# Kernel tuning notes

Measured on AMD Instinct MI355X. Metric: run time of the kernel, lower is better.

The kernel has to match this reference:

```python
import jax, jax.numpy as jnp
import numpy as np

H, C = 5, 128          # heads, hidden_channels
NUM_GRAPHS = 500
N_NODES, N_EDGES = 20000, 320000


def gat_layer(x, edge_attr, src, dst, W, We, a_src, a_dst, a_edge, b):
    """PyG GATConv with edge_dim, add_self_loops=True, fill_value='mean', concat heads."""
    N = x.shape[0]
    ed = edge_attr.dtype
    # self-loop edge_attr = scatter-mean of incoming edge_attr per target node
    deg = jax.ops.segment_sum(jnp.ones((dst.shape[0],), ed), dst, num_segments=N)
    loop_attr = jax.ops.segment_sum(edge_attr, dst, num_segments=N) / jnp.maximum(deg, 1.0)[:, None]
    loop = jnp.arange(N, dtype=src.dtype)
    s = jnp.concatenate([src, loop])
    d = jnp.concatenate([dst, loop])
    ea = jnp.concatenate([edge_attr, loop_attr], axis=0)
    h = (x @ W).reshape(N, H, C)            # [N,H,C]
    e = (ea @ We).reshape(-1, H, C)         # [E2,H,C]
    a_l = (h * a_src).sum(-1)               # [N,H]
    a_r = (h * a_dst).sum(-1)               # [N,H]
    a_e = (e * a_edge).sum(-1)              # [E2,H]
    alpha = jax.nn.leaky_relu(a_l[s] + a_r[d] + a_e, 0.2)
    # segment softmax over destination neighborhoods
    amax = jax.ops.segment_max(alpha, d, num_segments=N)
    ex = jnp.exp(alpha - amax[d])
    denom = jax.ops.segment_sum(ex, d, num_segments=N)
    att = ex / (denom[d] + 1e-16)           # [E2,H]
    msg = h[s] * att[..., None]             # [E2,H,C]
    out = jax.ops.segment_sum(msg, d, num_segments=N).reshape(N, H * C)
    return out + b


def setup_inputs() -> dict:
    key = jax.random.key(0)
    ks = jax.random.split(key, 24)
    p = lambda k, sh: (jax.random.normal(k, sh, dtype=jnp.float32) * 0.05)
    inp = {
        "x": jax.random.normal(ks[0], (N_NODES, 43), dtype=jnp.float32),
        "edge_attr": jax.random.normal(ks[1], (N_EDGES, 10), dtype=jnp.float32),
        "W1": p(ks[2], (43, H * C)),   "We1": p(ks[3], (10, H * C)),
        "asrc1": p(ks[4], (H, C)), "adst1": p(ks[5], (H, C)), "aedge1": p(ks[6], (H, C)),
        "b1": jnp.zeros((H * C,), jnp.float32),
        "W2": p(ks[7], (H * C, H * C)), "We2": p(ks[8], (10, H * C)),
        "asrc2": p(ks[9], (H, C)), "adst2": p(ks[10], (H, C)), "aedge2": p(ks[11], (H, C)),
        "b2": jnp.zeros((H * C,), jnp.float32),
        "W3": p(ks[12], (H * C, H * C)), "We3": p(ks[13], (10, H * C)),
        "asrc3": p(ks[14], (H, C)), "adst3": p(ks[15], (H, C)), "aedge3": p(ks[16], (H, C)),
        "b3": jnp.zeros((H * C,), jnp.float32),
        "Wlin": p(ks[17], (H * C, 1)), "blin": jnp.zeros((1,), jnp.float32),
        "edge_index": jax.random.randint(ks[18], (2, N_EDGES), 0, N_NODES, dtype=jnp.int32),
        "batch": jnp.sort(jax.random.randint(ks[19], (N_NODES,), 0, NUM_GRAPHS, dtype=jnp.int32)),
    }
    return inp


def reference(x, edge_attr, W1, We1, asrc1, adst1, aedge1, b1,
              W2, We2, asrc2, adst2, aedge2, b2,
              W3, We3, asrc3, adst3, aedge3, b3,
              Wlin, blin, edge_index, batch):
    src, dst = edge_index[0], edge_index[1]
    h = jax.nn.relu(gat_layer(x, edge_attr, src, dst, W1, We1, asrc1, adst1, aedge1, b1))
    h = jax.nn.relu(gat_layer(h, edge_attr, src, dst, W2, We2, asrc2, adst2, aedge2, b2))
    h = gat_layer(h, edge_attr, src, dst, W3, We3, asrc3, adst3, aedge3, b3)
    # global mean pool over graphs
    cnt = jax.ops.segment_sum(jnp.ones((h.shape[0],), h.dtype), batch, num_segments=NUM_GRAPHS)
    pooled = jax.ops.segment_sum(h, batch, num_segments=NUM_GRAPHS) / jnp.maximum(cnt, 1.0)[:, None]
    return (pooled @ Wlin + blin).squeeze(-1)   # [NUM_GRAPHS]
```

## Files before the change

### kernel.cpp

```cpp
#include <hip/hip_runtime.h>

#define N_NODESC 20000
#define N_EDGESC 320000
#define HC 640
#define NGRAPH 500

typedef unsigned short u16;
typedef unsigned int u32;
typedef __attribute__((ext_vector_type(8))) short bf16x8;
typedef __attribute__((ext_vector_type(4))) float f32x4;

__device__ __forceinline__ float wred_sum(float v){
  #pragma unroll
  for(int o=32;o;o>>=1) v += __shfl_xor(v,o,64);
  return v;
}
__device__ __forceinline__ float lrelu(float x){ return x>0.f? x:0.2f*x; }

__device__ __forceinline__ u16 f2bf(float f){
  u32 u=__float_as_uint(f);
  u32 r=u+0x7FFFu+((u>>16)&1u);
  return (u16)(r>>16);
}
__device__ __forceinline__ float bf2f(u16 s){ return __uint_as_float(((u32)s)<<16); }
__device__ __forceinline__ float bflo(u32 w){ return __uint_as_float(w<<16); }
__device__ __forceinline__ float bfhi(u32 w){ return __uint_as_float(w&0xFFFF0000u); }

__device__ __forceinline__ void gload16(const void* g, void* l){
  __builtin_amdgcn_global_load_lds((const __attribute__((address_space(1))) void*)g,
                                   (__attribute__((address_space(3))) void*)l, 16, 0, 0);
}


__global__ void k_count(const int* __restrict__ dst, int* __restrict__ cnt){
  int i=blockIdx.x*blockDim.x+threadIdx.x;
  if(i>=N_EDGESC) return;
  atomicAdd(&cnt[dst[i]],1);
}

__global__ void k_scan(const int* __restrict__ cnt, int* __restrict__ rptr, int* __restrict__ pos){
  __shared__ int ps[1024];
  int t=threadIdx.x;
  const int CH=20;
  int beg=t*CH, end=min(beg+CH, N_NODESC);
  int s=0;
  for(int i=beg;i<end;i++) s+=cnt[i];
  ps[t]=s; __syncthreads();
  for(int off=1;off<1024;off<<=1){
    int v=(t>=off)? ps[t-off]:0;
    __syncthreads();
    ps[t]+=v;
    __syncthreads();
  }
  int base=ps[t]-s;
  for(int i=beg;i<end;i++){ rptr[i]=base; pos[i]=base; base+=cnt[i]; }
}

__global__ void k_scatter(const int* __restrict__ dst, int* __restrict__ pos,
                          int* __restrict__ eidx, int* __restrict__ dstC){
  int i=blockIdx.x*blockDim.x+threadIdx.x;
  if(i>=N_EDGESC) return;
  int d=dst[i];
  int j=atomicAdd(&pos[d],1);
  eidx[j]=i;
  dstC[j]=d;
}

__global__ void k_csr_edges(const int* __restrict__ eidx, const int* __restrict__ src,
                            const float* __restrict__ eattr,
                            int* __restrict__ srcE, float* __restrict__ eattrC){
  int j=blockIdx.x*blockDim.x+threadIdx.x;
  if(j>=N_EDGESC) return;
  int e=eidx[j];
  srcE[j]=src[e];
  const float* ep=&eattr[(size_t)e*10];
  float* op=&eattrC[(size_t)j*10];
  #pragma unroll
  for(int k=0;k<10;k++) op[k]=ep[k];
}

__global__ __launch_bounds__(256) void k_loop_attr(const float* __restrict__ eattrC,
    const int* __restrict__ rptr, const int* __restrict__ cnt,
    float* __restrict__ lattr){
  int tid=threadIdx.x, lane=tid&63;
  int n=blockIdx.x*4+(tid>>6);
  if(n>=N_NODESC) return;
  int beg=rptr[n], deg=cnt[n];
  float s[10]={0,0,0,0,0,0,0,0,0,0};
  for(int off=lane; off<deg; off+=64){
    const float* ep=&eattrC[(size_t)(beg+off)*10];
    #pragma unroll
    for(int k=0;k<10;k++) s[k]+=ep[k];
  }
  float inv=1.f/fmaxf((float)deg,1.f);
  #pragma unroll
  for(int k=0;k<10;k++){
    float tot=wred_sum(s[k]);
    if(lane==0) lattr[(size_t)n*10+k]=tot*inv;
  }
}


__global__ void k_conv_x(const float* __restrict__ x, u16* __restrict__ hi, u16* __restrict__ lo){
  int idx=blockIdx.x*blockDim.x+threadIdx.x;
  if(idx>=N_NODESC*64) return;
  int n=idx>>6, kk=idx&63;
  float v = kk<43 ? x[n*43+kk] : 0.f;
  u16 h=f2bf(v);
  hi[idx]=h; lo[idx]=f2bf(v-bf2f(h));
}

__global__ void k_conv_w3(const float* __restrict__ W0, const float* __restrict__ W1,
                          const float* __restrict__ W2,
                          u16* __restrict__ hi, u16* __restrict__ lo){
  const int R0=HC*64, R1=R0+HC*HC;
  const int TOT=R1+HC*HC;
  int idx=blockIdx.x*blockDim.x+threadIdx.x;
  if(idx>=TOT) return;
  const float* W; int local, KP, KL, base;
  if(idx<R0){ W=W0; local=idx; KP=64; KL=43; base=0; }
  else if(idx<R1){ W=W1; local=idx-R0; KP=HC; KL=HC; base=R0; }
  else { W=W2; local=idx-R1; KP=HC; KL=HC; base=R1; }
  int n=local/KP, kk=local-n*KP;
  float v = kk<KL ? W[(size_t)kk*HC+n] : 0.f;
  u16 h=f2bf(v);
  hi[base+local]=h;
  lo[base+local]=f2bf(v-bf2f(h));
}


__global__ void k_ve3(const float* __restrict__ We0, const float* __restrict__ ae0,
                      const float* __restrict__ We1, const float* __restrict__ ae1,
                      const float* __restrict__ We2, const float* __restrict__ ae2,
                      float* __restrict__ ve3){
  int t=threadIdx.x;
  if(t>=150) return;
  int L=t/50, r=t-50*L, k=r/5, h=r%5;
  const float* We = (L==0)?We0:(L==1)?We1:We2;
  const float* ae = (L==0)?ae0:(L==1)?ae1:ae2;
  float s=0.f;
  for(int c=0;c<128;c++) s += We[k*HC + h*128 + c]*ae[h*128+c];
  ve3[t]=s;
}

__global__ void k_cb(const float* __restrict__ bias, const float* __restrict__ wlin,
                     float* __restrict__ cb){
  int lane=threadIdx.x;
  float s=0.f;
  for(int c=lane;c<HC;c+=64) s+=bias[c]*wlin[c];
  s=wred_sum(s);
  if(lane==0) cb[0]=s;
}

__global__ __launch_bounds__(256) void k_edge_terms3(const float* __restrict__ eattrC,
    const float* __restrict__ lattr, const float* __restrict__ ve3,
    float* __restrict__ aeC3, float* __restrict__ ael3){
  __shared__ float ves[150];
  if(threadIdx.x<150) ves[threadIdx.x]=ve3[threadIdx.x];
  __syncthreads();
  const int NEDGET=N_EDGESC+N_NODESC*5;
  int idx=blockIdx.x*blockDim.x+threadIdx.x;
  if(idx>=3*NEDGET) return;
  int L=idx/NEDGET, r=idx-L*NEDGET;
  const float* vl=&ves[L*50];
  if(r<N_EDGESC){
    float ev[10];
    const float* ep=&eattrC[(size_t)r*10];
    #pragma unroll
    for(int k=0;k<10;k++) ev[k]=ep[k];
    #pragma unroll
    for(int hh=0;hh<5;hh++){
      float s=0.f;
      #pragma unroll
      for(int k=0;k<10;k++) s+=ev[k]*vl[k*5+hh];
      aeC3[(size_t)L*N_EDGESC*5 + (size_t)r*5+hh]=s;
    }
  }else{
    int t=r-N_EDGESC;
    int n=t/5, h=t-5*n;
    float s=0.f;
    #pragma unroll
    for(int k=0;k<10;k++) s+=lattr[(size_t)n*10+k]*vl[k*5+h];
    ael3[(size_t)L*N_NODESC*5 + t]=s;
  }
}

__global__ void k_edgew(const int* __restrict__ srcE, const int* __restrict__ dstC,
                        const float* __restrict__ al, const float* __restrict__ ar,
                        const float* __restrict__ aeC, float* __restrict__ wE){
  int j=blockIdx.x*blockDim.x+threadIdx.x;
  if(j>=N_EDGESC) return;
  int s=srcE[j], d=dstC[j];
  const float* av=&aeC[(size_t)j*5];
  float* wp=&wE[(size_t)j*5];
  #pragma unroll
  for(int h=0;h<5;h++)
    wp[h]=__expf(lrelu(al[s*5+h]+ar[d*5+h]+av[h]));
}


template<int NT, bool HB, bool QOUT>
__global__ __launch_bounds__(256,(NT==1)?5:3) void k_gemm_fused(
    const u16* __restrict__ Ahi, const u16* __restrict__ Alo,
    const u16* __restrict__ Bhi, const u16* __restrict__ Blo,
    const float* __restrict__ asrc, const float* __restrict__ adst,
    const float* __restrict__ wlin,
    u16* __restrict__ hb, float* __restrict__ al, float* __restrict__ ar,
    float* __restrict__ qn,
    int M, int KP, int nblk){
  constexpr int TERMS=(NT==3)?4:2;
  constexpr int BOFF =(NT==3)?8192:4096;
  __shared__ u16 lds[2*TERMS*4096];
  int tid=threadIdx.x;
  int lane=tid&63;
  int w=tid>>6;
  int l15=lane&15, lg=lane>>4;
  int orig=blockIdx.x;
  int q=nblk>>3, r=nblk&7;
  int xcd=orig&7, off=orig>>3;
  int wg=(xcd<r? xcd*(q+1) : r*(q+1)+(xcd-r)*q)+off;
  int by=wg/5, bx=wg-5*by;
  int row0=by*128, col0=bx*128;
  int wr=w>>1, wc=w&1;

  f32x4 zero = {0.f,0.f,0.f,0.f};
  f32x4 acc[4][4];
  #pragma unroll
  for(int i=0;i<4;i++)
    #pragma unroll
    for(int j=0;j<4;j++) acc[i][j]=zero;

  auto stage=[&](int b, int k0){
    u16* base = lds + b*TERMS*4096;
    #pragma unroll
    for(int c=0;c<2;c++){
      int sb=w+4*c;
      int col=k0+lg*8;
      size_t aoff=(size_t)(row0+sb*16+l15)*KP + col;
      size_t boff=(size_t)(col0+sb*16+l15)*KP + col;
      gload16(Ahi+aoff, base + sb*512);
      if constexpr(NT==3) gload16(Alo+aoff, base+4096 + sb*512);
      gload16(Bhi+boff, base+BOFF + sb*512);
      if constexpr(NT==3) gload16(Blo+boff, base+BOFF+4096 + sb*512);
    }
  };

  int nt=KP/32;
  stage(0,0);
  __syncthreads();
  int cur=0;
  for(int t=0;t<nt;t++){
    if(t+1<nt) stage(cur^1,(t+1)*32);
    u16* cb = lds + cur*TERMS*4096;
    bf16x8 ah[4], bh[4];
    #pragma unroll
    for(int i=0;i<4;i++){
      ah[i]=*(const bf16x8*)&cb[(wr*4+i)*512 + lane*8];
      bh[i]=*(const bf16x8*)&cb[BOFF+(wc*4+i)*512 + lane*8];
    }
    if constexpr(NT==3){
      bf16x8 alv[4], bl[4];
      #pragma unroll
      for(int i=0;i<4;i++){
        alv[i]=*(const bf16x8*)&cb[4096+(wr*4+i)*512+lane*8];
        bl[i] =*(const bf16x8*)&cb[BOFF+4096+(wc*4+i)*512+lane*8];
      }
      #pragma unroll
      for(int i=0;i<4;i++)
        #pragma unroll
        for(int j=0;j<4;j++){
          acc[i][j]=__builtin_amdgcn_mfma_f32_16x16x32_bf16(ah[i], bh[j],acc[i][j],0,0,0);
          acc[i][j]=__builtin_amdgcn_mfma_f32_16x16x32_bf16(alv[i],bh[j],acc[i][j],0,0,0);
          acc[i][j]=__builtin_amdgcn_mfma_f32_16x16x32_bf16(ah[i], bl[j],acc[i][j],0,0,0);
        }
    }else{
      #pragma unroll
      for(int i=0;i<4;i++)
        #pragma unroll
        for(int j=0;j<4;j++)
          acc[i][j]=__builtin_amdgcn_mfma_f32_16x16x32_bf16(ah[i],bh[j],acc[i][j],0,0,0);
    }
    __syncthreads();
    cur^=1;
  }

  float asv[4], adv[4], wlv[4];
  #pragma unroll
  for(int j=0;j<4;j++){
    int c=col0+wc*64+j*16+l15;
    asv[j]=asrc[c]; adv[j]=adst[c];
    if(QOUT) wlv[j]=wlin[c];
  }
  if(HB){
    #pragma unroll
    for(int i=0;i<4;i++){
      #pragma unroll
      for(int j=0;j<4;j++){
        #pragma unroll
        for(int rr=0;rr<4;rr++){
          int row=row0+wr*64+i*16+lg*4+rr;
          if(row<M) hb[(size_t)row*HC + (j*16+l15)*10 + bx*2+wc]=f2bf(acc[i][j][rr]);
        }
      }
    }
  }
  float* redAl=(float*)lds;
  float* redAr=redAl+256;
  float* redQ =redAr+256;
  #pragma unroll
  for(int i=0;i<4;i++){
    #pragma unroll
    for(int rr=0;rr<4;rr++){
      float sa=0.f, sd=0.f, sq=0.f;
      #pragma unroll
      for(int j=0;j<4;j++){
        sa+=acc[i][j][rr]*asv[j];
        sd+=acc[i][j][rr]*adv[j];
        if(QOUT) sq+=acc[i][j][rr]*wlv[j];
      }
      #pragma unroll
      for(int o=1;o<16;o<<=1){
        sa+=__shfl_xor(sa,o,64); sd+=__shfl_xor(sd,o,64);
        if(QOUT) sq+=__shfl_xor(sq,o,64);
      }
      if(l15==0){
        int lr=wr*64+i*16+lg*4+rr;
        redAl[lr*2+wc]=sa; redAr[lr*2+wc]=sd;
        if(QOUT) redQ[lr*2+wc]=sq;
      }
    }
  }
  __syncthreads();
  if(tid<128){
    int row=row0+tid;
    if(row<M){
      al[(size_t)row*5+bx]=redAl[tid*2]+redAl[tid*2+1];
      ar[(size_t)row*5+bx]=redAr[tid*2]+redAr[tid*2+1];
      if(QOUT) qn[(size_t)row*5+bx]=redQ[tid*2]+redQ[tid*2+1];
    }
  }
}

__global__ __launch_bounds__(256) void k_agg(const u16* __restrict__ hb, const int* __restrict__ srcE,
    const int* __restrict__ rptr, const int* __restrict__ cnt,
    const float* __restrict__ al, const float* __restrict__ ar, const float* __restrict__ ael,
    const float* __restrict__ wE, const float* __restrict__ bias,
    u16* __restrict__ ohi){
  int tid=threadIdx.x, lane=tid&63;
  int n=blockIdx.x*4+(tid>>6);
  if(n>=N_NODESC) return;
  float den[5], acc[10];
  #pragma unroll
  for(int h=0;h<5;h++)
    den[h]=__expf(lrelu(al[n*5+h]+ar[n*5+h]+ael[n*5+h]));
  {
    const u32* sp=(const u32*)(hb+(size_t)n*HC+lane*10);
    #pragma unroll
    for(int j2=0;j2<5;j2++){
      u32 wv=sp[j2];
      acc[2*j2]  =den[j2]*bflo(wv);
      acc[2*j2+1]=den[j2]*bfhi(wv);
    }
  }
  int beg=rptr[n], end=beg+cnt[n];
  int j=beg;
  for(; j+3<end; j+=4){
    int sj[4];
    #pragma unroll
    for(int u=0;u<4;u++) sj[u]=srcE[j+u];
    float w[4][5];
    #pragma unroll
    for(int u=0;u<4;u++){
      const float* wp=&wE[(size_t)(j+u)*5];
      #pragma unroll
      for(int h=0;h<5;h++) w[u][h]=wp[h];
    }
    u32 wv[4][5];
    #pragma unroll
    for(int u=0;u<4;u++){
      const u32* hr=(const u32*)(hb+(size_t)sj[u]*HC+lane*10);
      #pragma unroll
      for(int j2=0;j2<5;j2++) wv[u][j2]=hr[j2];
    }
    #pragma unroll
    for(int u=0;u<4;u++){
      #pragma unroll
      for(int j2=0;j2<5;j2++){
        den[j2]+=w[u][j2]*0.2f;
      }
    }
    #pragma unroll
    for(int u=0;u<4;u++){
      #pragma unroll
      for(int j2=0;j2<5;j2++){
        den[j2]-=w[u][j2]*0.2f;
        den[j2]+=w[u][j2];
      }
    }
    #pragma unroll
    for(int u=0;u<4;u++){
      #pragma unroll
      for(int j2=0;j2<5;j2++){
        acc[2*j2]  +=w[u][j2]*bflo(wv[u][j2]);
        acc[2*j2+1]+=w[u][j2]*bfhi(wv[u][j2]);
      }
    }
  }
  for(; j<end; j++){
    int sj=srcE[j];
    const float* wp=&wE[(size_t)j*5];
    float w[5];
    #pragma unroll
    for(int h=0;h<5;h++){ w[h]=wp[h]; den[h]+=w[h]; }
    const u32* hr=(const u32*)(hb+(size_t)sj*HC+lane*10);
    #pragma unroll
    for(int j2=0;j2<5;j2++){
      u32 wv=hr[j2];
      acc[2*j2]  +=w[j2]*bflo(wv);
      acc[2*j2+1]+=w[j2]*bfhi(wv);
    }
  }
  #pragma unroll
  for(int k=0;k<10;k++){
    int ccol=lane+64*k;
    float vv=acc[k]/(den[k>>1]+1e-16f)+bias[ccol];
    vv=fmaxf(vv,0.f);
    ohi[(size_t)n*HC+ccol]=f2bf(vv);
  }
}

__global__ __launch_bounds__(256) void k_agg_last(const float* __restrict__ qn,
    const int* __restrict__ srcE, const int* __restrict__ rptr, const int* __restrict__ cnt,
    const float* __restrict__ al, const float* __restrict__ ar, const float* __restrict__ ael,
    const float* __restrict__ aeC, const float* __restrict__ cb,
    float* __restrict__ pnode){
  int tid=threadIdx.x;
  int sub=tid&15;
  int n=blockIdx.x*16+(tid>>4);
  if(n>=N_NODESC) return;
  float arn[5], den[5], qs[5];
  #pragma unroll
  for(int h=0;h<5;h++) arn[h]=ar[n*5+h];
  #pragma unroll
  for(int h=0;h<5;h++){ den[h]=0.f; qs[h]=0.f; }
  if(sub==0){
    #pragma unroll
    for(int h=0;h<5;h++){
      float pp=__expf(lrelu(al[n*5+h]+arn[h]+ael[n*5+h]));
      den[h]=pp; qs[h]=pp*qn[(size_t)n*5+h];
    }
  }
  int beg=rptr[n], deg=cnt[n];
  for(int off=sub; off<deg; off+=16){
    int j=beg+off;
    int s=srcE[j];
    const float* av=&aeC[(size_t)j*5];
    const float* qv=&qn[(size_t)s*5];
    #pragma unroll
    for(int h=0;h<5;h++){
      float pp=__expf(lrelu(al[s*5+h]+arn[h]+av[h]));
      den[h]+=pp; qs[h]+=pp*qv[h];
    }
  }
  #pragma unroll
  for(int h=0;h<5;h++){
    #pragma unroll
    for(int o=1;o<16;o<<=1){
      den[h]+=__shfl_xor(den[h],o,16);
      qs[h]+=__shfl_xor(qs[h],o,16);
    }
  }
  if(sub==0){
    float s=0.f;
    #pragma unroll
    for(int h=0;h<5;h++) s+=qs[h]/(den[h]+1e-16f);
    pnode[n]=s+cb[0];
  }
}

__global__ __launch_bounds__(256) void k_graphout(const float* __restrict__ pnode,
    const int* __restrict__ batch, const float* __restrict__ blin,
    float* __restrict__ out){
  int tid=threadIdx.x, lane=tid&63;
  int g=blockIdx.x*4+(tid>>6);
  if(g>=NGRAPH) return;
  auto lb=[&](int val){
    int lo=0, hi=N_NODESC;
    while(lo<hi){ int mid=(lo+hi)>>1; if(batch[mid]<val) lo=mid+1; else hi=mid; }
    return lo;
  };
  int s0=lb(g), s1=lb(g+1);
  float s=0.f;
  for(int i=s0+lane;i<s1;i+=64) s+=pnode[i];
  s=wred_sum(s);
  if(lane==0) out[g]=s/fmaxf((float)(s1-s0),1.f)+blin[0];
}


extern "C" void kernel_launch(void* const* d_in, const int* in_sizes, int n_in,
                              void* d_out, int out_size, void* d_ws, size_t ws_size,
                              hipStream_t stream){
  const float* x     = (const float*)d_in[0];
  const float* eattr = (const float*)d_in[1];
  const float* W[3]    ={(const float*)d_in[2],(const float*)d_in[8],(const float*)d_in[14]};
  const float* We[3]   ={(const float*)d_in[3],(const float*)d_in[9],(const float*)d_in[15]};
  const float* asrc[3] ={(const float*)d_in[4],(const float*)d_in[10],(const float*)d_in[16]};
  const float* adst[3] ={(const float*)d_in[5],(const float*)d_in[11],(const float*)d_in[17]};
  const float* aedge[3]={(const float*)d_in[6],(const float*)d_in[12],(const float*)d_in[18]};
  const float* bias[3] ={(const float*)d_in[7],(const float*)d_in[13],(const float*)d_in[19]};
  const float* Wlin  = (const float*)d_in[20];
  const float* blin  = (const float*)d_in[21];
  const int* eind    = (const int*)d_in[22];
  const int* srcp    = eind;
  const int* dstp    = eind + N_EDGESC;
  const int* batch   = (const int*)d_in[23];
  float* out = (float*)d_out;

  char* ws=(char*)d_ws;
  size_t o=0;
  auto alloc=[&](size_t bytes)->void*{ void* p=ws+o; o=(o+bytes+255)&~(size_t)255; return p; };
  u16* hb   =(u16*)alloc((size_t)N_NODESC*HC*2);
  u16* Ahi =(u16*)alloc((size_t)N_NODESC*HC*2);
  u16* Axhi=(u16*)alloc((size_t)N_NODESC*64*2);
  u16* Axlo=(u16*)alloc((size_t)N_NODESC*64*2);
  const int WB0=0, WB1=HC*64, WB2=WB1+HC*HC;
  u16* Bthi3=(u16*)alloc((size_t)(WB2+HC*HC)*2);
  u16* Btlo3=(u16*)alloc((size_t)(WB2+HC*HC)*2);
  float* al   =(float*)alloc((size_t)N_NODESC*5*4);
  float* ar   =(float*)alloc((size_t)N_NODESC*5*4);
  float* qn   =(float*)alloc((size_t)N_NODESC*5*4);
  float* ael3 =(float*)alloc((size_t)3*N_NODESC*5*4);
  float* aeC3 =(float*)alloc((size_t)3*N_EDGESC*5*4);
  float* wE   =(float*)alloc((size_t)N_EDGESC*5*4);
  float* lattr=(float*)alloc((size_t)N_NODESC*10*4);
  float* eattrC=(float*)alloc((size_t)N_EDGESC*10*4);
  float* ve3  =(float*)alloc(256*4);
  float* cbv  =(float*)alloc(64*4);
  float* pnode=(float*)alloc((size_t)N_NODESC*4);
  int* cntI   =(int*)alloc((size_t)N_NODESC*4);
  int* rptr   =(int*)alloc((size_t)N_NODESC*4);
  int* pos    =(int*)alloc((size_t)N_NODESC*4);
  int* eidx   =(int*)alloc((size_t)N_EDGESC*4);
  int* srcE   =(int*)alloc((size_t)N_EDGESC*4);
  int* dstC   =(int*)alloc((size_t)N_EDGESC*4);

  hipMemsetAsync(cntI,0,(size_t)N_NODESC*4,stream);

  k_count<<<(N_EDGESC+255)/256,256,0,stream>>>(dstp,cntI);
  k_scan<<<1,1024,0,stream>>>(cntI,rptr,pos);
  k_scatter<<<(N_EDGESC+255)/256,256,0,stream>>>(dstp,pos,eidx,dstC);
  k_csr_edges<<<(N_EDGESC+255)/256,256,0,stream>>>(eidx,srcp,eattr,srcE,eattrC);
  k_loop_attr<<<(N_NODESC+3)/4,256,0,stream>>>(eattrC,rptr,cntI,lattr);
  k_conv_x<<<(N_NODESC*64+255)/256,256,0,stream>>>(x,Axhi,Axlo);
  k_ve3<<<1,256,0,stream>>>(We[0],aedge[0],We[1],aedge[1],We[2],aedge[2],ve3);
  k_cb<<<1,64,0,stream>>>(bias[2],Wlin,cbv);
  {
    int tot=WB2+HC*HC;
    k_conv_w3<<<(tot+255)/256,256,0,stream>>>(W[0],W[1],W[2],Bthi3,Btlo3);
  }
  {
    const int NEDGET=N_EDGESC+N_NODESC*5;
    k_edge_terms3<<<(3*NEDGET+255)/256,256,0,stream>>>(eattrC,lattr,ve3,aeC3,ael3);
  }

  const int NBLK=5*((N_NODESC+127)/128);
  const int WBo[3]={WB0,WB1,WB2};
  for(int L=0;L<3;L++){
    int KP = (L==0)? 64 : HC;
    const float* aeL = aeC3 + (size_t)L*N_EDGESC*5;
    const float* aelL= ael3 + (size_t)L*N_NODESC*5;
    if(L==0){
      k_gemm_fused<3,true,false><<<NBLK,256,0,stream>>>(Axhi,Axlo,Bthi3+WBo[L],Btlo3+WBo[L],
          asrc[L],adst[L],Wlin,hb,al,ar,qn,N_NODESC,KP,NBLK);
      k_edgew<<<(N_EDGESC+255)/256,256,0,stream>>>(srcE,dstC,al,ar,aeL,wE);
      k_agg<<<(N_NODESC+3)/4,256,0,stream>>>(hb,srcE,rptr,cntI,al,ar,aelL,wE,bias[L],Ahi);
    }else if(L==1){
      k_gemm_fused<1,true,false><<<NBLK,256,0,stream>>>(Ahi,(const u16*)nullptr,Bthi3+WBo[L],(const u16*)nullptr,
          asrc[L],adst[L],Wlin,hb,al,ar,qn,N_NODESC,KP,NBLK);
      k_edgew<<<(N_EDGESC+255)/256,256,0,stream>>>(srcE,dstC,al,ar,aeL,wE);
      k_agg<<<(N_NODESC+3)/4,256,0,stream>>>(hb,srcE,rptr,cntI,al,ar,aelL,wE,bias[L],Ahi);
    }else{
      k_gemm_fused<1,false,true><<<NBLK,256,0,stream>>>(Ahi,(const u16*)nullptr,Bthi3+WBo[L],(const u16*)nullptr,
          asrc[L],adst[L],Wlin,hb,al,ar,qn,N_NODESC,KP,NBLK);
      k_agg_last<<<(N_NODESC+15)/16,256,0,stream>>>(qn,srcE,rptr,cntI,al,ar,aelL,aeL,cbv,pnode);
    }
  }
  k_graphout<<<(NGRAPH+3)/4,256,0,stream>>>(pnode,batch,blin,out);
}
```

Baseline: 443.0 us.

## Use 64-row GEMM tiles for layers 2-3 and simplify agg denominator update

Layers 2 and 3 switch from 128x128 tiles to a new 64x128-tile GEMM kernel, with each of the four waves computing a 64x32 slab. This doubles the block count for better occupancy and load balance across CUs, at the cost of more B-tile reloads per output. The layer-0 split-precision GEMM is kept as its own non-template kernel. In k_agg, a redundant add/subtract of 0.2*w on the denominator is removed and the unrolled loops are merged.

```diff
diff --git a/kernel.cpp b/kernel.cpp
--- a/kernel.cpp
+++ b/kernel.cpp
@@ -199,17 +199,14 @@
 }
 
 
-template<int NT, bool HB, bool QOUT>
-__global__ __launch_bounds__(256,(NT==1)?5:3) void k_gemm_fused(
+__global__ __launch_bounds__(256,3) void k_gemm_l0(
     const u16* __restrict__ Ahi, const u16* __restrict__ Alo,
     const u16* __restrict__ Bhi, const u16* __restrict__ Blo,
     const float* __restrict__ asrc, const float* __restrict__ adst,
-    const float* __restrict__ wlin,
     u16* __restrict__ hb, float* __restrict__ al, float* __restrict__ ar,
-    float* __restrict__ qn,
     int M, int KP, int nblk){
-  constexpr int TERMS=(NT==3)?4:2;
-  constexpr int BOFF =(NT==3)?8192:4096;
+  constexpr int TERMS=4;
+  constexpr int BOFF =8192;
   __shared__ u16 lds[2*TERMS*4096];
   int tid=threadIdx.x;
   int lane=tid&63;
@@ -239,9 +236,9 @@
       size_t aoff=(size_t)(row0+sb*16+l15)*KP + col;
       size_t boff=(size_t)(col0+sb*16+l15)*KP + col;
       gload16(Ahi+aoff, base + sb*512);
-      if constexpr(NT==3) gload16(Alo+aoff, base+4096 + sb*512);
+      gload16(Alo+aoff, base+4096 + sb*512);
       gload16(Bhi+boff, base+BOFF + sb*512);
-      if constexpr(NT==3) gload16(Blo+boff, base+BOFF+4096 + sb*512);
+      gload16(Blo+boff, base+BOFF+4096 + sb*512);
     }
   };
 
@@ -252,81 +249,57 @@
   for(int t=0;t<nt;t++){
     if(t+1<nt) stage(cur^1,(t+1)*32);
     u16* cb = lds + cur*TERMS*4096;
-    bf16x8 ah[4], bh[4];
+    bf16x8 ah[4], bh[4], alv[4], bl[4];
     #pragma unroll
     for(int i=0;i<4;i++){
       ah[i]=*(const bf16x8*)&cb[(wr*4+i)*512 + lane*8];
       bh[i]=*(const bf16x8*)&cb[BOFF+(wc*4+i)*512 + lane*8];
-    }
-    if constexpr(NT==3){
-      bf16x8 alv[4], bl[4];
-      #pragma unroll
-      for(int i=0;i<4;i++){
-        alv[i]=*(const bf16x8*)&cb[4096+(wr*4+i)*512+lane*8];
-        bl[i] =*(const bf16x8*)&cb[BOFF+4096+(wc*4+i)*512+lane*8];
-      }
-      #pragma unroll
-      for(int i=0;i<4;i++)
-        #pragma unroll
-        for(int j=0;j<4;j++){
-          acc[i][j]=__builtin_amdgcn_mfma_f32_16x16x32_bf16(ah[i], bh[j],acc[i][j],0,0,0);
-          acc[i][j]=__builtin_amdgcn_mfma_f32_16x16x32_bf16(alv[i],bh[j],acc[i][j],0,0,0);
-          acc[i][j]=__builtin_amdgcn_mfma_f32_16x16x32_bf16(ah[i], bl[j],acc[i][j],0,0,0);
-        }
-    }else{
-      #pragma unroll
-      for(int i=0;i<4;i++)
-        #pragma unroll
-        for(int j=0;j<4;j++)
-          acc[i][j]=__builtin_amdgcn_mfma_f32_16x16x32_bf16(ah[i],bh[j],acc[i][j],0,0,0);
-    }
+      alv[i]=*(const bf16x8*)&cb[4096+(wr*4+i)*512+lane*8];
+      bl[i] =*(const bf16x8*)&cb[BOFF+4096+(wc*4+i)*512+lane*8];
+    }
+    #pragma unroll
+    for(int i=0;i<4;i++)
+      #pragma unroll
+      for(int j=0;j<4;j++){
+        acc[i][j]=__builtin_amdgcn_mfma_f32_16x16x32_bf16(ah[i], bh[j],acc[i][j],0,0,0);
+        acc[i][j]=__builtin_amdgcn_mfma_f32_16x16x32_bf16(alv[i],bh[j],acc[i][j],0,0,0);
+        acc[i][j]=__builtin_amdgcn_mfma_f32_16x16x32_bf16(ah[i], bl[j],acc[i][j],0,0,0);
+      }
     __syncthreads();
     cur^=1;
   }
 
-  float asv[4], adv[4], wlv[4];
+  float asv[4], adv[4];
   #pragma unroll
   for(int j=0;j<4;j++){
     int c=col0+wc*64+j*16+l15;
     asv[j]=asrc[c]; adv[j]=adst[c];
-    if(QOUT) wlv[j]=wlin[c];
-  }
-  if(HB){
-    #pragma unroll
-    for(int i=0;i<4;i++){
-      #pragma unroll
-      for(int j=0;j<4;j++){
-        #pragma unroll
-        for(int rr=0;rr<4;rr++){
-          int row=row0+wr*64+i*16+lg*4+rr;
-          if(row<M) hb[(size_t)row*HC + (j*16+l15)*10 + bx*2+wc]=f2bf(acc[i][j][rr]);
-        }
+  }
+  #pragma unroll
+  for(int i=0;i<4;i++){
+    #pragma unroll
+    for(int j=0;j<4;j++){
+      #pragma unroll
+      for(int rr=0;rr<4;rr++){
+        int row=row0+wr*64+i*16+lg*4+rr;
+        if(row<M) hb[(size_t)row*HC + (j*16+l15)*10 + bx*2+wc]=f2bf(acc[i][j][rr]);
       }
     }
   }
   float* redAl=(float*)lds;
   float* redAr=redAl+256;
-  float* redQ =redAr+256;
   #pragma unroll
   for(int i=0;i<4;i++){
     #pragma unroll
     for(int rr=0;rr<4;rr++){
-      float sa=0.f, sd=0.f, sq=0.f;
-      #pragma unroll
-      for(int j=0;j<4;j++){
-        sa+=acc[i][j][rr]*asv[j];
-        sd+=acc[i][j][rr]*adv[j];
-        if(QOUT) sq+=acc[i][j][rr]*wlv[j];
-      }
-      #pragma unroll
-      for(int o=1;o<16;o<<=1){
-        sa+=__shfl_xor(sa,o,64); sd+=__shfl_xor(sd,o,64);
-        if(QOUT) sq+=__shfl_xor(sq,o,64);
-      }
+      float sa=0.f, sd=0.f;
+      #pragma unroll
+      for(int j=0;j<4;j++){ sa+=acc[i][j][rr]*asv[j]; sd+=acc[i][j][rr]*adv[j]; }
+      #pragma unroll
+      for(int o=1;o<16;o<<=1){ sa+=__shfl_xor(sa,o,64); sd+=__shfl_xor(sd,o,64); }
       if(l15==0){
         int lr=wr*64+i*16+lg*4+rr;
         redAl[lr*2+wc]=sa; redAr[lr*2+wc]=sd;
-        if(QOUT) redQ[lr*2+wc]=sq;
       }
     }
   }
@@ -336,7 +309,124 @@
     if(row<M){
       al[(size_t)row*5+bx]=redAl[tid*2]+redAl[tid*2+1];
       ar[(size_t)row*5+bx]=redAr[tid*2]+redAr[tid*2+1];
-      if(QOUT) qn[(size_t)row*5+bx]=redQ[tid*2]+redQ[tid*2+1];
+    }
+  }
+}
+
+template<bool HB, bool QOUT>
+__global__ __launch_bounds__(256,6) void k_gemm64(
+    const u16* __restrict__ A,
+    const u16* __restrict__ B,
+    const float* __restrict__ asrc, const float* __restrict__ adst,
+    const float* __restrict__ wlin,
+    u16* __restrict__ hb, float* __restrict__ al, float* __restrict__ ar,
+    float* __restrict__ qn,
+    int M, int KP, int nblk){
+  __shared__ u16 lds[2*6144];
+  int tid=threadIdx.x;
+  int lane=tid&63;
+  int w=tid>>6;
+  int l15=lane&15, lg=lane>>4;
+  int orig=blockIdx.x;
+  int q=nblk>>3, r=nblk&7;
+  int xcd=orig&7, off=orig>>3;
+  int wg=(xcd<r? xcd*(q+1) : r*(q+1)+(xcd-r)*q)+off;
+  int by=wg/5, bx=wg-5*by;
+  int row0=by*64, col0=bx*128;
+
+  f32x4 zero = {0.f,0.f,0.f,0.f};
+  f32x4 acc[4][2];
+  #pragma unroll
+  for(int i=0;i<4;i++){ acc[i][0]=zero; acc[i][1]=zero; }
+
+  auto stage=[&](int b, int k0){
+    u16* base = lds + b*6144;
+    int colk=k0+lg*8;
+    size_t aoff=(size_t)(row0+w*16+l15)*KP + colk;
+    gload16(A+aoff, base + w*512);
+    #pragma unroll
+    for(int c=0;c<2;c++){
+      int sb=w+4*c;
+      size_t boff=(size_t)(col0+sb*16+l15)*KP + colk;
+      gload16(B+boff, base+2048 + sb*512);
+    }
+  };
+
+  int nt=KP/32;
+  stage(0,0);
+  __syncthreads();
+  int cur=0;
+  for(int t=0;t<nt;t++){
+    if(t+1<nt) stage(cur^1,(t+1)*32);
+    u16* cb = lds + cur*6144;
+    bf16x8 ah[4], bh[2];
+    #pragma unroll
+    for(int i=0;i<4;i++) ah[i]=*(const bf16x8*)&cb[i*512 + lane*8];
+    #pragma unroll
+    for(int j=0;j<2;j++) bh[j]=*(const bf16x8*)&cb[2048+(w*2+j)*512 + lane*8];
+    #pragma unroll
+    for(int i=0;i<4;i++){
+      acc[i][0]=__builtin_amdgcn_mfma_f32_16x16x32_bf16(ah[i],bh[0],acc[i][0],0,0,0);
+      acc[i][1]=__builtin_amdgcn_mfma_f32_16x16x32_bf16(ah[i],bh[1],acc[i][1],0,0,0);
+    }
+    __syncthreads();
+    cur^=1;
+  }
+
+  float asv[2], adv[2], wlv[2];
+  #pragma unroll
+  for(int j=0;j<2;j++){
+    int c=col0+w*32+j*16+l15;
+    asv[j]=asrc[c]; adv[j]=adst[c];
+    if(QOUT) wlv[j]=wlin[c];
+  }
+  if(HB){
+    #pragma unroll
+    for(int i=0;i<4;i++){
+      #pragma unroll
+      for(int j=0;j<2;j++){
+        #pragma unroll
+        for(int rr=0;rr<4;rr++){
+          int row=row0+i*16+lg*4+rr;
+          if(row<M)
+            hb[(size_t)row*HC + ((w&1)*32+j*16+l15)*10 + bx*2+(w>>1)]=f2bf(acc[i][j][rr]);
+        }
+      }
+    }
+  }
+  float* redAl=(float*)lds;
+  float* redAr=redAl+256;
+  float* redQ =redAr+256;
+  #pragma unroll
+  for(int i=0;i<4;i++){
+    #pragma unroll
+    for(int rr=0;rr<4;rr++){
+      float sa=0.f, sd=0.f, sq=0.f;
+      #pragma unroll
+      for(int j=0;j<2;j++){
+        sa+=acc[i][j][rr]*asv[j];
+        sd+=acc[i][j][rr]*adv[j];
+        if(QOUT) sq+=acc[i][j][rr]*wlv[j];
+      }
+      #pragma unroll
+      for(int o=1;o<16;o<<=1){
+        sa+=__shfl_xor(sa,o,64); sd+=__shfl_xor(sd,o,64);
+        if(QOUT) sq+=__shfl_xor(sq,o,64);
+      }
+      if(l15==0){
+        int lr=i*16+lg*4+rr;
+        redAl[lr*4+w]=sa; redAr[lr*4+w]=sd;
+        if(QOUT) redQ[lr*4+w]=sq;
+      }
+    }
+  }
+  __syncthreads();
+  if(tid<64){
+    int row=row0+tid;
+    if(row<M){
+      al[(size_t)row*5+bx]=redAl[tid*4]+redAl[tid*4+1]+redAl[tid*4+2]+redAl[tid*4+3];
+      ar[(size_t)row*5+bx]=redAr[tid*4]+redAr[tid*4+1]+redAr[tid*4+2]+redAr[tid*4+3];
+      if(QOUT) qn[(size_t)row*5+bx]=redQ[tid*4]+redQ[tid*4+1]+redQ[tid*4+2]+redQ[tid*4+3];
     }
   }
 }
@@ -386,21 +476,7 @@
     for(int u=0;u<4;u++){
       #pragma unroll
       for(int j2=0;j2<5;j2++){
-        den[j2]+=w[u][j2]*0.2f;
-      }
-    }
-    #pragma unroll
-    for(int u=0;u<4;u++){
-      #pragma unroll
-      for(int j2=0;j2<5;j2++){
-        den[j2]-=w[u][j2]*0.2f;
         den[j2]+=w[u][j2];
-      }
-    }
-    #pragma unroll
-    for(int u=0;u<4;u++){
-      #pragma unroll
-      for(int j2=0;j2<5;j2++){
         acc[2*j2]  +=w[u][j2]*bflo(wv[u][j2]);
         acc[2*j2+1]+=w[u][j2]*bfhi(wv[u][j2]);
       }
@@ -563,25 +639,24 @@
     k_edge_terms3<<<(3*NEDGET+255)/256,256,0,stream>>>(eattrC,lattr,ve3,aeC3,ael3);
   }
 
-  const int NBLK=5*((N_NODESC+127)/128);
-  const int WBo[3]={WB0,WB1,WB2};
+  const int NBLK0=5*((N_NODESC+127)/128);
+  const int NBLK64=5*((N_NODESC+63)/64);
   for(int L=0;L<3;L++){
-    int KP = (L==0)? 64 : HC;
     const float* aeL = aeC3 + (size_t)L*N_EDGESC*5;
     const float* aelL= ael3 + (size_t)L*N_NODESC*5;
     if(L==0){
-      k_gemm_fused<3,true,false><<<NBLK,256,0,stream>>>(Axhi,Axlo,Bthi3+WBo[L],Btlo3+WBo[L],
-          asrc[L],adst[L],Wlin,hb,al,ar,qn,N_NODESC,KP,NBLK);
+      k_gemm_l0<<<NBLK0,256,0,stream>>>(Axhi,Axlo,Bthi3+WB0,Btlo3+WB0,
+          asrc[L],adst[L],hb,al,ar,N_NODESC,64,NBLK0);
       k_edgew<<<(N_EDGESC+255)/256,256,0,stream>>>(srcE,dstC,al,ar,aeL,wE);
       k_agg<<<(N_NODESC+3)/4,256,0,stream>>>(hb,srcE,rptr,cntI,al,ar,aelL,wE,bias[L],Ahi);
     }else if(L==1){
-      k_gemm_fused<1,true,false><<<NBLK,256,0,stream>>>(Ahi,(const u16*)nullptr,Bthi3+WBo[L],(const u16*)nullptr,
-          asrc[L],adst[L],Wlin,hb,al,ar,qn,N_NODESC,KP,NBLK);
+      k_gemm64<true,false><<<NBLK64,256,0,stream>>>(Ahi,Bthi3+WB1,
+          asrc[L],adst[L],Wlin,hb,al,ar,qn,N_NODESC,HC,NBLK64);
       k_edgew<<<(N_EDGESC+255)/256,256,0,stream>>>(srcE,dstC,al,ar,aeL,wE);
       k_agg<<<(N_NODESC+3)/4,256,0,stream>>>(hb,srcE,rptr,cntI,al,ar,aelL,wE,bias[L],Ahi);
     }else{
-      k_gemm_fused<1,false,true><<<NBLK,256,0,stream>>>(Ahi,(const u16*)nullptr,Bthi3+WBo[L],(const u16*)nullptr,
-          asrc[L],adst[L],Wlin,hb,al,ar,qn,N_NODESC,KP,NBLK);
+      k_gemm64<false,true><<<NBLK64,256,0,stream>>>(Ahi,Bthi3+WB2,
+          asrc[L],adst[L],Wlin,hb,al,ar,qn,N_NODESC,HC,NBLK64);
       k_agg_last<<<(N_NODESC+15)/16,256,0,stream>>>(qn,srcE,rptr,cntI,al,ar,aelL,aeL,cbv,pnode);
     }
   }
```

After: 446.1 us. Within noise of the previous version (+0.7%).
